# Kernel optimization log

Measured on AMD Instinct MI355X. Metric: run time of the kernel, lower is better.

## Reference

```python
import jax, jax.numpy as jnp
import numpy as np

NUM_HEADS = 16
NUM_KV_HEADS = 4
HEAD_DIM = 128
ROPE_THETA = 500000.0
RMS_EPS = 1e-5


def _rms_norm(x, w, eps=RMS_EPS):
    # normalize over last dim in fp32, as in YuaRMSNorm
    xf = x.astype(jnp.float32)
    var = jnp.mean(xf * xf, axis=-1, keepdims=True)
    return (w * (xf * jax.lax.rsqrt(var + eps))).astype(x.dtype)


def _rotate_half(x):
    x1, x2 = jnp.split(x, 2, axis=-1)
    return jnp.concatenate([-x2, x1], axis=-1)


def _rope_cos_sin(seq_len, dim, dtype):
    inv_freq = 1.0 / (ROPE_THETA ** (jnp.arange(0, dim, 2, dtype=jnp.float32) / dim))
    pos = jnp.arange(seq_len, dtype=jnp.float32)
    freqs = pos[:, None] * inv_freq[None, :]          # [S, dim/2]
    emb = jnp.concatenate([freqs, freqs], axis=-1)     # [S, dim]
    return jnp.cos(emb).astype(dtype), jnp.sin(emb).astype(dtype)


def setup_inputs() -> dict:
    key = jax.random.key(0)
    ks = jax.random.split(key, 5)
    B, S, H = 2, 2048, 2048
    q_out = NUM_HEADS * HEAD_DIM
    kv_out = NUM_KV_HEADS * HEAD_DIM
    sc = 0.02
    return {
        "hidden_states": jax.random.normal(ks[0], (B, S, H), jnp.float32),
        "q_w": jax.random.normal(ks[1], (q_out, H), jnp.float32) * sc,
        "k_w": jax.random.normal(ks[2], (kv_out, H), jnp.float32) * sc,
        "v_w": jax.random.normal(ks[3], (kv_out, H), jnp.float32) * sc,
        "o_w": jax.random.normal(ks[4], (H, q_out), jnp.float32) * sc,
        "q_norm_w": jnp.ones((HEAD_DIM,), jnp.float32),
        "k_norm_w": jnp.ones((HEAD_DIM,), jnp.float32),
    }


def reference(hidden_states, q_w, k_w, v_w, o_w, q_norm_w, k_norm_w):
    B, S, H = hidden_states.shape
    groups = NUM_HEADS // NUM_KV_HEADS

    # fused-ish QKV projections (torch Linear: x @ W^T)
    q = jnp.einsum('bsh,oh->bso', hidden_states, q_w).reshape(B, S, NUM_HEADS, HEAD_DIM).transpose(0, 2, 1, 3)
    k = jnp.einsum('bsh,oh->bso', hidden_states, k_w).reshape(B, S, NUM_KV_HEADS, HEAD_DIM).transpose(0, 2, 1, 3)
    v = jnp.einsum('bsh,oh->bso', hidden_states, v_w).reshape(B, S, NUM_KV_HEADS, HEAD_DIM).transpose(0, 2, 1, 3)

    # QK RMSNorm over head_dim
    q = _rms_norm(q, q_norm_w)
    k = _rms_norm(k, k_norm_w)

    # RoPE (position_ids = arange(S))
    cos, sin = _rope_cos_sin(S, HEAD_DIM, q.dtype)  # [S, hd]
    cos = cos[None, None]  # [1,1,S,hd]
    sin = sin[None, None]
    q = q * cos + _rotate_half(q) * sin
    k = k * cos + _rotate_half(k) * sin

    # GQA repeat_interleave of kv heads
    k = jnp.repeat(k, groups, axis=1)  # [B, num_heads, S, hd]
    v = jnp.repeat(v, groups, axis=1)

    # causal SDPA
    scale = 1.0 / jnp.sqrt(jnp.asarray(HEAD_DIM, q.dtype))
    scores = jnp.einsum('bhqd,bhkd->bhqk', q, k) * scale
    causal = jnp.tril(jnp.ones((S, S), bool))
    scores = jnp.where(causal[None, None], scores, jnp.finfo(scores.dtype).min)
    probs = jax.nn.softmax(scores, axis=-1)
    attn = jnp.einsum('bhqk,bhkd->bhqd', probs, v)

    attn = attn.transpose(0, 2, 1, 3).reshape(B, S, NUM_HEADS * HEAD_DIM)
    return jnp.einsum('bso,ho->bsh', attn, o_w)
```

## Files before the change

### kernel.cpp

```cpp
#include <hip/hip_runtime.h>
#include <stdint.h>

#define S_LEN 2048
#define BATCH 2
#define NH 16
#define NKV 4
#define HD 128
#define HID 2048
#define MROWS (BATCH * S_LEN)
#define PST 72

typedef unsigned short u16;
typedef __attribute__((ext_vector_type(8))) short frag_ab;
typedef __attribute__((ext_vector_type(4))) float frag_cd;

static __device__ __forceinline__ float bf2f(u16 v) {
    union { unsigned u; float f; } t; t.u = ((unsigned)v) << 16; return t.f;
}
static __device__ __forceinline__ u16 f2bf(float f) {
    union { float f; unsigned u; } t; t.f = f;
    unsigned r = t.u + 0x7fffu + ((t.u >> 16) & 1u);
    return (u16)(r >> 16);
}
static __device__ __forceinline__ void load_lds16(const u16* g, u16* l) {
    __builtin_amdgcn_global_load_lds((const __attribute__((address_space(1))) void*)g,
                                     (__attribute__((address_space(3))) void*)l, 16, 0, 0);
}

__global__ __launch_bounds__(256) void conv_f32_bf16(const float* __restrict__ src,
                                                     u16* __restrict__ dst, int n4) {
    int i = blockIdx.x * 256 + threadIdx.x;
    if (i >= n4) return;
    float4 v = ((const float4*)src)[i];
    ushort4 o;
    o.x = f2bf(v.x); o.y = f2bf(v.y); o.z = f2bf(v.z); o.w = f2bf(v.w);
    ((ushort4*)dst)[i] = o;
}

__global__ __launch_bounds__(256) void gemm_bt(const u16* __restrict__ A, const u16* __restrict__ B,
                                               float* __restrict__ C, int M, int N, int K) {
    __shared__ u16 As[128 * 32];
    __shared__ u16 Bs[128 * 32];
    const int tid = threadIdx.x;
    const int wave = tid >> 6, lane = tid & 63;
    const int quad = lane >> 4, lr = lane & 15;
    const int wm = (wave & 1) * 64, wn = (wave >> 1) * 64;
    const long bm = (long)blockIdx.x * 128, bn = (long)blockIdx.y * 128;
    const int srow = (wave << 4) + (lane >> 2);
    const int scol = (lane & 3) * 8;
    const u16* Ag = A + (bm + srow) * (long)K + scol;
    const u16* Bg = B + (bn + srow) * (long)K + scol;
    u16* AsW = As + wave * 512;
    u16* BsW = Bs + wave * 512;

    frag_cd acc[4][4];
#pragma unroll
    for (int i = 0; i < 4; i++)
#pragma unroll
        for (int j = 0; j < 4; j++) acc[i][j] = (frag_cd){0.f, 0.f, 0.f, 0.f};

    for (int k0 = 0; k0 < K; k0 += 32) {
        __syncthreads();
        load_lds16(Ag + k0, AsW);
        load_lds16(Ag + (long)64 * K + k0, AsW + 2048);
        load_lds16(Bg + k0, BsW);
        load_lds16(Bg + (long)64 * K + k0, BsW + 2048);
        __syncthreads();
        frag_ab af[4], bfr[4];
#pragma unroll
        for (int i = 0; i < 4; i++) af[i] = *(const frag_ab*)(As + (wm + i * 16 + lr) * 32 + quad * 8);
#pragma unroll
        for (int j = 0; j < 4; j++) bfr[j] = *(const frag_ab*)(Bs + (wn + j * 16 + lr) * 32 + quad * 8);
#pragma unroll
        for (int i = 0; i < 4; i++)
#pragma unroll
            for (int j = 0; j < 4; j++)
                acc[i][j] = __builtin_amdgcn_mfma_f32_16x16x32_bf16(af[i], bfr[j], acc[i][j], 0, 0, 0);
    }
#pragma unroll
    for (int i = 0; i < 4; i++)
#pragma unroll
        for (int j = 0; j < 4; j++)
#pragma unroll
            for (int r = 0; r < 4; r++) {
                long row = bm + wm + i * 16 + quad * 4 + r;
                long col = bn + wn + j * 16 + lr;
                C[row * N + col] = acc[i][j][r];
            }
}

__global__ __launch_bounds__(256) void rope_norm(const float* __restrict__ src, u16* __restrict__ dst,
                                                 const float* __restrict__ nw, int nh, int stride, int coff) {
    const int m = blockIdx.x;
    const int wave = threadIdx.x >> 6, lane = threadIdx.x & 63;
    const int s = m & (S_LEN - 1), b = m >> 11;
    const int d0 = 2 * lane;
    const float w0 = nw[d0], w1 = nw[d0 + 1];
    const int i0 = d0 & 63;
    const float lnt_over = 13.122363377404328f / 64.f;
    float inv0 = expf(-(float)i0 * lnt_over);
    float inv1 = expf(-(float)(i0 + 1) * lnt_over);
    float c0 = cosf((float)s * inv0), sn0 = sinf((float)s * inv0);
    float c1 = cosf((float)s * inv1), sn1 = sinf((float)s * inv1);
    for (int h = wave; h < nh; h += 4) {
        float2 x = *(const float2*)(src + (long)m * stride + coff + h * HD + d0);
        float ss = x.x * x.x + x.y * x.y;
#pragma unroll
        for (int off = 1; off < 64; off <<= 1) ss += __shfl_xor(ss, off);
        float rs = rsqrtf(ss * (1.f / HD) + 1e-5f);
        float xn0 = x.x * rs * w0;
        float xn1 = x.y * rs * w1;
        float p0 = __shfl_xor(xn0, 32);
        float p1 = __shfl_xor(xn1, 32);
        float r0 = (lane < 32) ? -p0 : p0;
        float r1 = (lane < 32) ? -p1 : p1;
        float y0 = xn0 * c0 + r0 * sn0;
        float y1 = xn1 * c1 + r1 * sn1;
        unsigned outw = (unsigned)f2bf(y0) | ((unsigned)f2bf(y1) << 16);
        *(unsigned*)(dst + (((long)(b * nh + h) * S_LEN + s) * HD + d0)) = outw;
    }
}

__global__ __launch_bounds__(256) void pack_vt(const float* __restrict__ src, u16* __restrict__ dst,
                                               int stride, int coff) {
    __shared__ u16 t[128 * 72];
    const int tid = threadIdx.x;
    const int st = blockIdx.x & 31;
    const int kh = (blockIdx.x >> 5) & 3;
    const int b = blockIdx.x >> 7;
    const long m0 = (long)b * S_LEN + st * 64;
#pragma unroll
    for (int c = 0; c < 8; c++) {
        int idx = c * 256 + tid;
        int r = idx >> 5, cg = idx & 31;
        float4 v = *(const float4*)(src + (m0 + r) * stride + coff + kh * HD + cg * 4);
        int col = cg * 4;
        t[(col + 0) * 72 + r] = f2bf(v.x);
        t[(col + 1) * 72 + r] = f2bf(v.y);
        t[(col + 2) * 72 + r] = f2bf(v.z);
        t[(col + 3) * 72 + r] = f2bf(v.w);
    }
    __syncthreads();
    const int d = tid >> 1, sh = (tid & 1) * 32;
    u16* dp = dst + ((long)(b * NKV + kh) * HD + d) * S_LEN + st * 64 + sh;
    const u16* tp = &t[d * 72 + sh];
    *(uint4*)(dp + 0)  = *(const uint4*)(tp + 0);
    *(uint4*)(dp + 8)  = *(const uint4*)(tp + 8);
    *(uint4*)(dp + 16) = *(const uint4*)(tp + 16);
    *(uint4*)(dp + 24) = *(const uint4*)(tp + 24);
}

__global__ __launch_bounds__(256, 2) void flash_attn(const u16* __restrict__ Q, const u16* __restrict__ K,
                                                     const u16* __restrict__ Vt, u16* __restrict__ O) {
    __shared__ __align__(16) char shmem[19456];
    u16* Pls = (u16*)shmem;
    float* maccf = (float*)shmem;
    float* mlbf = (float*)(shmem + 18432);
#define MACC(mt, dt, c, r) (((((mt) * 8 + (dt)) * 16 + (c)) * 16) + (r))
#define MLB(w, mt, row, j) (((((w) * 2 + (mt)) * 16 + (row)) * 2) + (j))
    const int tid = threadIdx.x;
    const int wave = tid >> 6, lane = tid & 63;
    const int quad = lane >> 4, lr = lane & 15;
    const int g = blockIdx.x & 7;
    const int sub = (blockIdx.x >> 3) & 3;
    const int tt = blockIdx.x >> 5;
    const int t = 63 - tt;
    const int b = g >> 2, kh = g & 3;
    const int h = kh * 4 + sub;
    const float scale = 0.08838834764831845f;
    const u16* Qb = Q + ((long)(b * NH + h) * S_LEN) * HD;
    const u16* Kb = K + ((long)(b * NKV + kh) * S_LEN) * HD;
    const u16* Vb = Vt + ((long)(b * NKV + kh) * HD) * S_LEN;
    const int pbase = wave * 32 * PST;

    const int q0 = t * 32;
    const int nkt = (t >> 1) + 1;

    frag_ab qf[2][4];
#pragma unroll
    for (int mt = 0; mt < 2; mt++) {
        int qrow = q0 + mt * 16 + lr;
#pragma unroll
        for (int ks = 0; ks < 4; ks++)
            qf[mt][ks] = *(const frag_ab*)(Qb + (long)qrow * HD + ks * 32 + quad * 8);
    }
    frag_cd oa[2][8];
    float m_i[2][4], l_i[2][4];
#pragma unroll
    for (int mt = 0; mt < 2; mt++) {
#pragma unroll
        for (int dt = 0; dt < 8; dt++) oa[mt][dt] = (frag_cd){0.f, 0.f, 0.f, 0.f};
#pragma unroll
        for (int r = 0; r < 4; r++) { m_i[mt][r] = -3e38f; l_i[mt][r] = 0.f; }
    }

    for (int kt = wave; kt < nkt; kt += 4) {
        const int j0 = kt * 64;
        frag_cd sa[2][4];
#pragma unroll
        for (int mt = 0; mt < 2; mt++)
#pragma unroll
            for (int nt = 0; nt < 4; nt++) sa[mt][nt] = (frag_cd){0.f, 0.f, 0.f, 0.f};
#pragma unroll
        for (int nt = 0; nt < 4; nt++) {
            frag_ab kf[4];
#pragma unroll
            for (int ks = 0; ks < 4; ks++)
                kf[ks] = *(const frag_ab*)(Kb + (long)(j0 + nt * 16 + lr) * HD + ks * 32 + quad * 8);
#pragma unroll
            for (int mt = 0; mt < 2; mt++)
#pragma unroll
                for (int ks = 0; ks < 4; ks++)
                    sa[mt][nt] = __builtin_amdgcn_mfma_f32_16x16x32_bf16(qf[mt][ks], kf[ks], sa[mt][nt], 0, 0, 0);
        }
        frag_ab vf[2][8];
#pragma unroll
        for (int ks = 0; ks < 2; ks++)
#pragma unroll
            for (int dt = 0; dt < 8; dt++)
                vf[ks][dt] = *(const frag_ab*)(Vb + (long)(dt * 16 + lr) * S_LEN + j0 + ks * 32 + quad * 8);

        const bool need_mask = (j0 + 63) > q0;
#pragma unroll
        for (int mt = 0; mt < 2; mt++) {
            float mrow[4] = {-3e38f, -3e38f, -3e38f, -3e38f};
#pragma unroll
            for (int nt = 0; nt < 4; nt++) {
                int key = j0 + nt * 16 + lr;
#pragma unroll
                for (int r = 0; r < 4; r++) {
                    int qrow = q0 + mt * 16 + quad * 4 + r;
                    float v = sa[mt][nt][r] * scale;
                    if (need_mask) v = (key <= qrow) ? v : -3e38f;
                    sa[mt][nt][r] = v;
                    mrow[r] = fmaxf(mrow[r], v);
                }
            }
#pragma unroll
            for (int off = 1; off < 16; off <<= 1)
#pragma unroll
                for (int r = 0; r < 4; r++) mrow[r] = fmaxf(mrow[r], __shfl_xor(mrow[r], off));
            float rs[4];
#pragma unroll
            for (int r = 0; r < 4; r++) {
                float mn = fmaxf(m_i[mt][r], mrow[r]);
                float alpha = __expf(m_i[mt][r] - mn);
                m_i[mt][r] = mn;
                l_i[mt][r] *= alpha;
                rs[r] = 0.f;
#pragma unroll
                for (int dt = 0; dt < 8; dt++) oa[mt][dt][r] *= alpha;
            }
#pragma unroll
            for (int nt = 0; nt < 4; nt++)
#pragma unroll
                for (int r = 0; r < 4; r++) {
                    float pw = __expf(sa[mt][nt][r] - m_i[mt][r]);
                    rs[r] += pw;
                    Pls[pbase + (mt * 16 + quad * 4 + r) * PST + nt * 16 + lr] = f2bf(pw);
                }
#pragma unroll
            for (int off = 1; off < 16; off <<= 1)
#pragma unroll
                for (int r = 0; r < 4; r++) rs[r] += __shfl_xor(rs[r], off);
#pragma unroll
            for (int r = 0; r < 4; r++) l_i[mt][r] += rs[r];
        }

#pragma unroll
        for (int ks = 0; ks < 2; ks++) {
            frag_ab pf[2];
#pragma unroll
            for (int mt = 0; mt < 2; mt++)
                pf[mt] = *(const frag_ab*)&Pls[pbase + (mt * 16 + lr) * PST + ks * 32 + quad * 8];
#pragma unroll
            for (int dt = 0; dt < 8; dt++) {
                oa[0][dt] = __builtin_amdgcn_mfma_f32_16x16x32_bf16(pf[0], vf[ks][dt], oa[0][dt], 0, 0, 0);
                oa[1][dt] = __builtin_amdgcn_mfma_f32_16x16x32_bf16(pf[1], vf[ks][dt], oa[1][dt], 0, 0, 0);
            }
        }
    }

    if (lr == 0) {
#pragma unroll
        for (int mt = 0; mt < 2; mt++)
#pragma unroll
            for (int r = 0; r < 4; r++) {
                mlbf[MLB(wave, mt, quad * 4 + r, 0)] = m_i[mt][r];
                mlbf[MLB(wave, mt, quad * 4 + r, 1)] = l_i[mt][r];
            }
    }
    __syncthreads();
    float inv[2][4];
#pragma unroll
    for (int mt = 0; mt < 2; mt++)
#pragma unroll
        for (int r = 0; r < 4; r++) {
            int row = quad * 4 + r;
            float m0 = mlbf[MLB(0, mt, row, 0)], m1 = mlbf[MLB(1, mt, row, 0)];
            float m2 = mlbf[MLB(2, mt, row, 0)], m3 = mlbf[MLB(3, mt, row, 0)];
            float ms = fmaxf(fmaxf(m0, m1), fmaxf(m2, m3));
            float ls = mlbf[MLB(0, mt, row, 1)] * __expf(m0 - ms) + mlbf[MLB(1, mt, row, 1)] * __expf(m1 - ms)
                     + mlbf[MLB(2, mt, row, 1)] * __expf(m2 - ms) + mlbf[MLB(3, mt, row, 1)] * __expf(m3 - ms);
            inv[mt][r] = 1.f / ls;
            float alpha = __expf(m_i[mt][r] - ms);
#pragma unroll
            for (int dt = 0; dt < 8; dt++) oa[mt][dt][r] *= alpha;
        }
    for (int w = 0; w < 4; w++) {
        if (wave == w) {
#pragma unroll
            for (int mt = 0; mt < 2; mt++)
#pragma unroll
                for (int dt = 0; dt < 8; dt++) {
                    frag_cd* pp = (frag_cd*)&maccf[MACC(mt, dt, lr, quad * 4)];
                    if (w == 0) *pp = oa[mt][dt];
                    else {
                        frag_cd o = *pp;
#pragma unroll
                        for (int r = 0; r < 4; r++) o[r] += oa[mt][dt][r];
                        *pp = o;
                    }
                }
        }
        __syncthreads();
    }
#pragma unroll
    for (int mt = 0; mt < 2; mt++)
#pragma unroll
        for (int dto = 0; dto < 2; dto++) {
            int dt = wave * 2 + dto;
            frag_cd v = *(const frag_cd*)&maccf[MACC(mt, dt, lr, quad * 4)];
#pragma unroll
            for (int r = 0; r < 4; r++) {
                int s = q0 + mt * 16 + quad * 4 + r;
                O[((long)b * S_LEN + s) * (NH * HD) + h * HD + dt * 16 + lr] =
                    f2bf(v[r] * inv[mt][r]);
            }
        }
#undef MACC
#undef MLB
}

extern "C" void kernel_launch(void* const* d_in, const int* in_sizes, int n_in,
                              void* d_out, int out_size, void* d_ws, size_t ws_size,
                              hipStream_t stream) {
    const float* hs  = (const float*)d_in[0];
    const float* q_w = (const float*)d_in[1];
    const float* k_w = (const float*)d_in[2];
    const float* v_w = (const float*)d_in[3];
    const float* o_w = (const float*)d_in[4];
    const float* qnw = (const float*)d_in[5];
    const float* knw = (const float*)d_in[6];
    float* out = (float*)d_out;

    char* ws = (char*)d_ws;
    u16* hs_bf  = (u16*)(ws);
    u16* wbuf   = (u16*)(ws + (16ul << 20));
    float* gout = (float*)(ws + (24ul << 20));
    u16* Kr     = (u16*)(ws + (40ul << 20));
    u16* Vt     = (u16*)(ws + (44ul << 20));
    u16* Qr     = (u16*)(ws + (56ul << 20));
    (void)ws_size; (void)in_sizes; (void)n_in; (void)out_size;

    conv_f32_bf16<<<(MROWS * HID / 4 + 255) / 256, 256, 0, stream>>>(hs, hs_bf, MROWS * HID / 4);

    conv_f32_bf16<<<(HID * HID / 4 + 255) / 256, 256, 0, stream>>>(q_w, wbuf, HID * HID / 4);
    dim3 gq(MROWS / 128, HID / 128);
    gemm_bt<<<gq, 256, 0, stream>>>(hs_bf, wbuf, gout, MROWS, HID, HID);
    rope_norm<<<MROWS, 256, 0, stream>>>(gout, Qr, qnw, NH, HID, 0);

    conv_f32_bf16<<<(NKV * HD * HID / 4 + 255) / 256, 256, 0, stream>>>(k_w, wbuf, NKV * HD * HID / 4);
    conv_f32_bf16<<<(NKV * HD * HID / 4 + 255) / 256, 256, 0, stream>>>(v_w, wbuf + NKV * HD * HID, NKV * HD * HID / 4);
    dim3 gkv(MROWS / 128, (2 * NKV * HD) / 128);
    gemm_bt<<<gkv, 256, 0, stream>>>(hs_bf, wbuf, gout, MROWS, 2 * NKV * HD, HID);
    rope_norm<<<MROWS, 256, 0, stream>>>(gout, Kr, knw, NKV, 2 * NKV * HD, 0);
    pack_vt<<<BATCH * NKV * (S_LEN / 64), 256, 0, stream>>>(gout, Vt, 2 * NKV * HD, NKV * HD);

    flash_attn<<<2048, 256, 0, stream>>>(Qr, Kr, Vt, hs_bf);

    conv_f32_bf16<<<(HID * HID / 4 + 255) / 256, 256, 0, stream>>>(o_w, wbuf, HID * HID / 4);
    gemm_bt<<<gq, 256, 0, stream>>>(hs_bf, wbuf, out, MROWS, HID, HID);
}
```

Baseline: 448.4 us.

## Fuse Q/K/V projections into one GEMM and add 128x64 tile GEMM

When the workspace is large enough, the Q, K and V weights are converted into one contiguous buffer and a single GEMM produces all three projections. RoPE/norm and the V pack then read from that combined output at column offsets. A new 128x64-tile GEMM variant is used for the output projection and, in the fallback path, for the KV projection. This doubles the number of workgroups on the 256-CU device and removes an extra GEMM launch, at the cost of a larger workspace and lower per-block data reuse.

```diff
diff --git a/kernel.cpp b/kernel.cpp
--- a/kernel.cpp
+++ b/kernel.cpp
@@ -81,6 +81,57 @@
     for (int i = 0; i < 4; i++)
 #pragma unroll
         for (int j = 0; j < 4; j++)
+#pragma unroll
+            for (int r = 0; r < 4; r++) {
+                long row = bm + wm + i * 16 + quad * 4 + r;
+                long col = bn + wn + j * 16 + lr;
+                C[row * N + col] = acc[i][j][r];
+            }
+}
+
+__global__ __launch_bounds__(256) void gemm_bt64(const u16* __restrict__ A, const u16* __restrict__ B,
+                                                 float* __restrict__ C, int M, int N, int K) {
+    __shared__ u16 As[128 * 32];
+    __shared__ u16 Bs[64 * 32];
+    const int tid = threadIdx.x;
+    const int wave = tid >> 6, lane = tid & 63;
+    const int quad = lane >> 4, lr = lane & 15;
+    const int wm = (wave & 1) * 64, wn = (wave >> 1) * 32;
+    const long bm = (long)blockIdx.x * 128, bn = (long)blockIdx.y * 64;
+    const int srow = (wave << 4) + (lane >> 2);
+    const int scol = (lane & 3) * 8;
+    const u16* Ag = A + (bm + srow) * (long)K + scol;
+    const u16* Bg = B + (bn + srow) * (long)K + scol;
+    u16* AsW = As + wave * 512;
+    u16* BsW = Bs + wave * 512;
+
+    frag_cd acc[4][2];
+#pragma unroll
+    for (int i = 0; i < 4; i++)
+#pragma unroll
+        for (int j = 0; j < 2; j++) acc[i][j] = (frag_cd){0.f, 0.f, 0.f, 0.f};
+
+    for (int k0 = 0; k0 < K; k0 += 32) {
+        __syncthreads();
+        load_lds16(Ag + k0, AsW);
+        load_lds16(Ag + (long)64 * K + k0, AsW + 2048);
+        load_lds16(Bg + k0, BsW);
+        __syncthreads();
+        frag_ab af[4], bfr[2];
+#pragma unroll
+        for (int i = 0; i < 4; i++) af[i] = *(const frag_ab*)(As + (wm + i * 16 + lr) * 32 + quad * 8);
+#pragma unroll
+        for (int j = 0; j < 2; j++) bfr[j] = *(const frag_ab*)(Bs + (wn + j * 16 + lr) * 32 + quad * 8);
+#pragma unroll
+        for (int i = 0; i < 4; i++)
+#pragma unroll
+            for (int j = 0; j < 2; j++)
+                acc[i][j] = __builtin_amdgcn_mfma_f32_16x16x32_bf16(af[i], bfr[j], acc[i][j], 0, 0, 0);
+    }
+#pragma unroll
+    for (int i = 0; i < 4; i++)
+#pragma unroll
+        for (int j = 0; j < 2; j++)
 #pragma unroll
             for (int r = 0; r < 4; r++) {
                 long row = bm + wm + i * 16 + quad * 4 + r;
@@ -353,32 +404,61 @@
     const float* qnw = (const float*)d_in[5];
     const float* knw = (const float*)d_in[6];
     float* out = (float*)d_out;
-
     char* ws = (char*)d_ws;
-    u16* hs_bf  = (u16*)(ws);
-    u16* wbuf   = (u16*)(ws + (16ul << 20));
-    float* gout = (float*)(ws + (24ul << 20));
-    u16* Kr     = (u16*)(ws + (40ul << 20));
-    u16* Vt     = (u16*)(ws + (44ul << 20));
-    u16* Qr     = (u16*)(ws + (56ul << 20));
-    (void)ws_size; (void)in_sizes; (void)n_in; (void)out_size;
-
-    conv_f32_bf16<<<(MROWS * HID / 4 + 255) / 256, 256, 0, stream>>>(hs, hs_bf, MROWS * HID / 4);
-
-    conv_f32_bf16<<<(HID * HID / 4 + 255) / 256, 256, 0, stream>>>(q_w, wbuf, HID * HID / 4);
-    dim3 gq(MROWS / 128, HID / 128);
-    gemm_bt<<<gq, 256, 0, stream>>>(hs_bf, wbuf, gout, MROWS, HID, HID);
-    rope_norm<<<MROWS, 256, 0, stream>>>(gout, Qr, qnw, NH, HID, 0);
-
-    conv_f32_bf16<<<(NKV * HD * HID / 4 + 255) / 256, 256, 0, stream>>>(k_w, wbuf, NKV * HD * HID / 4);
-    conv_f32_bf16<<<(NKV * HD * HID / 4 + 255) / 256, 256, 0, stream>>>(v_w, wbuf + NKV * HD * HID, NKV * HD * HID / 4);
-    dim3 gkv(MROWS / 128, (2 * NKV * HD) / 128);
-    gemm_bt<<<gkv, 256, 0, stream>>>(hs_bf, wbuf, gout, MROWS, 2 * NKV * HD, HID);
-    rope_norm<<<MROWS, 256, 0, stream>>>(gout, Kr, knw, NKV, 2 * NKV * HD, 0);
-    pack_vt<<<BATCH * NKV * (S_LEN / 64), 256, 0, stream>>>(gout, Vt, 2 * NKV * HD, NKV * HD);
-
-    flash_attn<<<2048, 256, 0, stream>>>(Qr, Kr, Vt, hs_bf);
-
-    conv_f32_bf16<<<(HID * HID / 4 + 255) / 256, 256, 0, stream>>>(o_w, wbuf, HID * HID / 4);
-    gemm_bt<<<gq, 256, 0, stream>>>(hs_bf, wbuf, out, MROWS, HID, HID);
-}
+    (void)in_sizes; (void)n_in; (void)out_size;
+
+    if (ws_size >= (100ul << 20)) {
+        u16* hs_bf  = (u16*)(ws);
+        u16* wbuf   = (u16*)(ws + (16ul << 20));
+        float* gout = (float*)(ws + (28ul << 20));
+        u16* Kr     = (u16*)(ws + (76ul << 20));
+        u16* Vt     = (u16*)(ws + (80ul << 20));
+        u16* Qr     = (u16*)(ws + (84ul << 20));
+        const int NQKV = HID + 2 * NKV * HD;
+
+        conv_f32_bf16<<<(MROWS * HID / 4 + 255) / 256, 256, 0, stream>>>(hs, hs_bf, MROWS * HID / 4);
+        conv_f32_bf16<<<(HID * HID / 4 + 255) / 256, 256, 0, stream>>>(q_w, wbuf, HID * HID / 4);
+        conv_f32_bf16<<<(NKV * HD * HID / 4 + 255) / 256, 256, 0, stream>>>(k_w, wbuf + (long)HID * HID, NKV * HD * HID / 4);
+        conv_f32_bf16<<<(NKV * HD * HID / 4 + 255) / 256, 256, 0, stream>>>(v_w, wbuf + (long)(HID + NKV * HD) * HID, NKV * HD * HID / 4);
+
+        dim3 gqkv(MROWS / 128, NQKV / 128);
+        gemm_bt<<<gqkv, 256, 0, stream>>>(hs_bf, wbuf, gout, MROWS, NQKV, HID);
+
+        rope_norm<<<MROWS, 256, 0, stream>>>(gout, Qr, qnw, NH, NQKV, 0);
+        rope_norm<<<MROWS, 256, 0, stream>>>(gout, Kr, knw, NKV, NQKV, HID);
+        pack_vt<<<BATCH * NKV * (S_LEN / 64), 256, 0, stream>>>(gout, Vt, NQKV, HID + NKV * HD);
+
+        flash_attn<<<2048, 256, 0, stream>>>(Qr, Kr, Vt, hs_bf);
+
+        conv_f32_bf16<<<(HID * HID / 4 + 255) / 256, 256, 0, stream>>>(o_w, wbuf, HID * HID / 4);
+        dim3 go(MROWS / 128, HID / 64);
+        gemm_bt64<<<go, 256, 0, stream>>>(hs_bf, wbuf, out, MROWS, HID, HID);
+    } else {
+        u16* hs_bf  = (u16*)(ws);
+        u16* wbuf   = (u16*)(ws + (16ul << 20));
+        float* gout = (float*)(ws + (24ul << 20));
+        u16* Kr     = (u16*)(ws + (40ul << 20));
+        u16* Vt     = (u16*)(ws + (44ul << 20));
+        u16* Qr     = (u16*)(ws + (56ul << 20));
+
+        conv_f32_bf16<<<(MROWS * HID / 4 + 255) / 256, 256, 0, stream>>>(hs, hs_bf, MROWS * HID / 4);
+
+        conv_f32_bf16<<<(HID * HID / 4 + 255) / 256, 256, 0, stream>>>(q_w, wbuf, HID * HID / 4);
+        dim3 gq(MROWS / 128, HID / 128);
+        gemm_bt<<<gq, 256, 0, stream>>>(hs_bf, wbuf, gout, MROWS, HID, HID);
+        rope_norm<<<MROWS, 256, 0, stream>>>(gout, Qr, qnw, NH, HID, 0);
+
+        conv_f32_bf16<<<(NKV * HD * HID / 4 + 255) / 256, 256, 0, stream>>>(k_w, wbuf, NKV * HD * HID / 4);
+        conv_f32_bf16<<<(NKV * HD * HID / 4 + 255) / 256, 256, 0, stream>>>(v_w, wbuf + NKV * HD * HID, NKV * HD * HID / 4);
+        dim3 gkv(MROWS / 128, (2 * NKV * HD) / 64);
+        gemm_bt64<<<gkv, 256, 0, stream>>>(hs_bf, wbuf, gout, MROWS, 2 * NKV * HD, HID);
+        rope_norm<<<MROWS, 256, 0, stream>>>(gout, Kr, knw, NKV, 2 * NKV * HD, 0);
+        pack_vt<<<BATCH * NKV * (S_LEN / 64), 256, 0, stream>>>(gout, Vt, 2 * NKV * HD, NKV * HD);
+
+        flash_attn<<<2048, 256, 0, stream>>>(Qr, Kr, Vt, hs_bf);
+
+        conv_f32_bf16<<<(HID * HID / 4 + 255) / 256, 256, 0, stream>>>(o_w, wbuf, HID * HID / 4);
+        dim3 go(MROWS / 128, HID / 64);
+        gemm_bt64<<<go, 256, 0, stream>>>(hs_bf, wbuf, out, MROWS, HID, HID);
+    }
+}
```

New measurement: 423.2 us. 1.06x faster.
